# Performance work log

Hardware: AMD Instinct MI355X
Metric: run time of the kernel (lower is better)

## Reference

```python
import jax, jax.numpy as jnp
import numpy as np

IN_CHANNELS = 128
N_NODES = 100000
N_EDGES = 625000


def setup_inputs() -> dict:
    key = jax.random.key(0)
    k1, k2, k3, k4, k5, k6 = jax.random.split(key, 6)
    d = IN_CHANNELS
    x = jax.random.normal(k1, (N_NODES, d), dtype=jnp.float32)
    edge_index = jax.random.randint(k2, (2, N_EDGES), 0, N_NODES, dtype=jnp.int64)
    # Linear params, torch default init: U(-1/sqrt(fan_in), 1/sqrt(fan_in))
    b1_bound = 1.0 / np.sqrt(2 * d)
    W1 = jax.random.uniform(k3, (d, 2 * d), minval=-b1_bound, maxval=b1_bound, dtype=jnp.float32)
    b1 = jax.random.uniform(k4, (d,), minval=-b1_bound, maxval=b1_bound, dtype=jnp.float32)
    b2_bound = 1.0 / np.sqrt(d)
    W2 = jax.random.uniform(k5, (1, d), minval=-b2_bound, maxval=b2_bound, dtype=jnp.float32)
    b2 = jax.random.uniform(k6, (1,), minval=-b2_bound, maxval=b2_bound, dtype=jnp.float32)
    return {"x": x, "edge_index": edge_index, "W1": W1, "b1": b1, "W2": W2, "b2": b2}


def reference(x, edge_index, W1, b1, W2, b2):
    # Gather endpoint features and concat along feature dim: [E, 2d]
    h = jnp.concatenate([x[edge_index[0]], x[edge_index[1]]], axis=1)
    h = jax.nn.relu(h @ W1.T + b1)          # [E, d]
    h = jax.nn.relu(h @ W2.T + b2)          # [E, 1]
    return jax.nn.sigmoid(h)
```

## Files before the change

### kernel.cpp

```cpp
#include <hip/hip_runtime.h>
#include <hip/hip_bf16.h>
#include <hip/hip_fp16.h>
#include <math.h>


typedef short    s16x4 __attribute__((ext_vector_type(4)));
typedef short    s16x8 __attribute__((ext_vector_type(8)));
typedef float    f32x4 __attribute__((ext_vector_type(4)));
typedef _Float16 h16x2 __attribute__((ext_vector_type(2)));

#define D    128
#define ALD  136

static __device__ inline short f2bf(float f) {
    unsigned u = __builtin_bit_cast(unsigned, f);
    unsigned r = (u + 0x7FFFu + ((u >> 16) & 1u)) >> 16;
    return (short)r;
}

static __device__ inline unsigned enc1_sw(float f) {
    f = fminf(fmaxf(f, -448.f), 448.f);
    unsigned short h = __builtin_bit_cast(unsigned short, (_Float16)(f * (1.0f / 256.0f)));
    unsigned s = (h >> 8) & 0x80u;
    unsigned mag = h & 0x7FFFu;
    mag = mag + 0x3Fu + ((mag >> 7) & 1u);
    return s | ((mag >> 7) & 0x7Fu);
}
static __device__ inline unsigned enc2(float a, float b) {
#if __has_builtin(__builtin_amdgcn_cvt_pk_fp8_f32)
    return ((unsigned)__builtin_amdgcn_cvt_pk_fp8_f32(a, b, 0, false)) & 0xFFFFu;
#else
    return enc1_sw(a) | (enc1_sw(b) << 8);
#endif
}

#if __has_builtin(__builtin_amdgcn_cvt_pk_f16_fp8)
#define YSC 1.0f
static __device__ inline h16x2 dec2lo(unsigned v) {
    return __builtin_amdgcn_cvt_pk_f16_fp8((short)v);
}
static __device__ inline h16x2 dec2hi(unsigned v) {
    return __builtin_amdgcn_cvt_pk_f16_fp8((short)(v >> 16));
}
#else
#define YSC 256.0f
static __device__ inline h16x2 dec2lo(unsigned v) {
    unsigned p = __builtin_amdgcn_perm(0u, v, 0x0C010C00u);
    unsigned h = ((p << 8) & 0x80008000u) | ((p << 7) & 0x3F803F80u);
    return __builtin_bit_cast(h16x2, h);
}
static __device__ inline h16x2 dec2hi(unsigned v) {
    unsigned p = __builtin_amdgcn_perm(0u, v, 0x0C030C02u);
    unsigned h = ((p << 8) & 0x80008000u) | ((p << 7) & 0x3F803F80u);
    return __builtin_bit_cast(h16x2, h);
}
#endif

static __device__ inline h16x2 reluh(h16x2 v) {
#if __has_builtin(__builtin_elementwise_max)
    h16x2 z = { (_Float16)0.0f, (_Float16)0.0f };
    return __builtin_elementwise_max(v, z);
#else
    unsigned u = __builtin_bit_cast(unsigned, v);
    unsigned m = ((u >> 15) & 0x00010001u) * 0xFFFFu;
    u &= ~m;
    return __builtin_bit_cast(h16x2, u);
#endif
}

static __device__ inline float dot2acc(h16x2 a, h16x2 b, float c) {
#if __has_builtin(__builtin_amdgcn_fdot2)
    return __builtin_amdgcn_fdot2(a, b, c, false);
#else
    return c + (float)a[0] * (float)b[0] + (float)a[1] * (float)b[1];
#endif
}

__global__ __launch_bounds__(256) void pack_w1_kernel(
    const float* __restrict__ W1, short* __restrict__ W1F)
{
    int g    = blockIdx.x * 256 + threadIdx.x;
    int lane = g & 63;
    int c    = (g >> 6) & 3;
    int j    = (g >> 8) & 3;
    int cs   = g >> 10;
    int o    = cs * 64 + j * 16 + (lane & 15);
    int kb   = c * 32 + (lane >> 4) * 8;
    const float* wp = W1 + (size_t)(o & 127) * 256 + (o >> 7) * 128 + kb;
    float4 u0 = *(const float4*)wp;
    float4 u1 = *(const float4*)(wp + 4);
    s16x8 v = { f2bf(u0.x), f2bf(u0.y), f2bf(u0.z), f2bf(u0.w),
                f2bf(u1.x), f2bf(u1.y), f2bf(u1.z), f2bf(u1.w) };
    *(s16x8*)&W1F[(size_t)g * 8] = v;
}

__global__ __launch_bounds__(256) void precompute_kernel(
    const float* __restrict__ x,
    const short* __restrict__ W1F,
    const float* __restrict__ b1,
    unsigned char* __restrict__ Y8,
    int N, int ntiles)
{
    __shared__ short At[2][32 * ALD];

    const int tid  = threadIdx.x;
    const int wid  = tid >> 6;
    const int lane = tid & 63;
    const int quad = lane >> 4, l15 = lane & 15;
    const int cs   = wid;

    s16x8 bf[4][4];
    #pragma unroll
    for (int j = 0; j < 4; ++j)
        #pragma unroll
        for (int c = 0; c < 4; ++c)
            bf[c][j] = *(const s16x8*)&W1F[(size_t)(((cs * 4 + j) * 4 + c) * 64 + lane) * 8];

    f32x4 b1v[4];
    #pragma unroll
    for (int j = 0; j < 4; ++j) {
        if (cs < 2) b1v[j] = *(const f32x4*)&b1[cs * 64 + j * 16 + quad * 4];
        else        b1v[j] = (f32x4){0.f, 0.f, 0.f, 0.f};
    }

    const int srow = tid >> 3;
    const int sc0  = (tid & 7) * 4;
    const int g    = gridDim.x;

    int t = blockIdx.x;
    float4 xv[4];
    {
        int m = t * 32 + srow; if (m >= N) m = N - 1;
        const float* xp = &x[(size_t)m * D + sc0];
        #pragma unroll
        for (int p = 0; p < 4; ++p)
            xv[p] = *(const float4*)(xp + p * 32);
    }
    #pragma unroll
    for (int p = 0; p < 4; ++p) {
        s16x4 bv = { f2bf(xv[p].x), f2bf(xv[p].y), f2bf(xv[p].z), f2bf(xv[p].w) };
        *(s16x4*)&At[0][srow * ALD + sc0 + p * 32] = bv;
    }
    __syncthreads();

    int buf = 0;
    while (t < ntiles) {
        const int tn = t + g;

        if (tn < ntiles) {
            int m = tn * 32 + srow; if (m >= N) m = N - 1;
            const float* xp = &x[(size_t)m * D + sc0];
            #pragma unroll
            for (int p = 0; p < 4; ++p)
                xv[p] = *(const float4*)(xp + p * 32);
        }

        f32x4 acc[2][4] = {};
        #pragma unroll
        for (int c = 0; c < 4; ++c) {
            s16x8 af[2];
            #pragma unroll
            for (int i = 0; i < 2; ++i)
                af[i] = *(const s16x8*)&At[buf][(i * 16 + l15) * ALD + c * 32 + quad * 8];
            #pragma unroll
            for (int i = 0; i < 2; ++i)
                #pragma unroll
                for (int j = 0; j < 4; ++j)
                    acc[i][j] = __builtin_amdgcn_mfma_f32_16x16x32_bf16(
                        bf[c][j], af[i], acc[i][j], 0, 0, 0);
        }

        const int m0 = t * 32;
        #pragma unroll
        for (int i = 0; i < 2; ++i) {
            int m = m0 + i * 16 + l15;
            if (m < N) {
                unsigned char* yp = Y8 + (size_t)m * 256 + cs * 64 + quad * 4;
                #pragma unroll
                for (int j = 0; j < 4; ++j) {
                    f32x4 v = acc[i][j] + b1v[j];
                    unsigned dw = enc2(v[0], v[1]) | (enc2(v[2], v[3]) << 16);
                    *(unsigned*)(yp + j * 16) = dw;
                }
            }
        }

        if (tn < ntiles) {
            #pragma unroll
            for (int p = 0; p < 4; ++p) {
                s16x4 bv = { f2bf(xv[p].x), f2bf(xv[p].y), f2bf(xv[p].z), f2bf(xv[p].w) };
                *(s16x4*)&At[buf ^ 1][srow * ALD + sc0 + p * 32] = bv;
            }
        }
        __syncthreads();
        buf ^= 1;
        t = tn;
    }
}

#define EPB 128

__global__ __launch_bounds__(256) void edge_kernel(
    const unsigned char* __restrict__ Y8,
    const int*           __restrict__ ei,
    const float*         __restrict__ W2,
    const float*         __restrict__ b2,
    float*               __restrict__ out,
    int E)
{
    const int tid = threadIdx.x;
    const int sub = tid & 7;
    const int grp = tid >> 3;
    const int e0  = blockIdx.x * EPB + grp;

    h16x2 w2h[8];
    {
        const float* wp = &W2[sub * 16];
        #pragma unroll
        for (int q = 0; q < 8; ++q) {
            float2 f = *(const float2*)(wp + q * 2);
            w2h[q] = (h16x2){ (_Float16)(f.x * YSC), (_Float16)(f.y * YSC) };
        }
    }

    int  ee[4]; bool vv[4]; uint4 L[4], R[4];
    #pragma unroll
    for (int k = 0; k < 4; ++k) {
        ee[k] = e0 + 32 * k;
        vv[k] = (ee[k] < E);
        int src = vv[k] ? ei[ee[k]] : 0;
        int dst = vv[k] ? ei[E + ee[k]] : 0;
        L[k] = *(const uint4*)(Y8 + (size_t)src * 256 + sub * 16);
        R[k] = *(const uint4*)(Y8 + (size_t)dst * 256 + 128 + sub * 16);
    }

    float s[4] = { 0.f, 0.f, 0.f, 0.f };
    #pragma unroll
    for (int k = 0; k < 4; ++k) {
        const unsigned* a = (const unsigned*)&L[k];
        const unsigned* c = (const unsigned*)&R[k];
        #pragma unroll
        for (int d = 0; d < 4; ++d) {
            h16x2 za = reluh(dec2lo(a[d]) + dec2lo(c[d]));
            s[k] = dot2acc(za, w2h[2*d],     s[k]);
            h16x2 zb = reluh(dec2hi(a[d]) + dec2hi(c[d]));
            s[k] = dot2acc(zb, w2h[2*d + 1], s[k]);
        }
    }

    #pragma unroll
    for (int k = 0; k < 4; ++k) {
        s[k] += __shfl_xor(s[k], 1);
        s[k] += __shfl_xor(s[k], 2);
        s[k] += __shfl_xor(s[k], 4);
    }

    if (sub == 0) {
        float bb = b2[0];
        #pragma unroll
        for (int k = 0; k < 4; ++k) {
            if (vv[k]) {
                float t = fmaxf(s[k] + bb, 0.f);
                out[ee[k]] = 1.0f / (1.0f + expf(-t));
            }
        }
    }
}

#define BM   128
#define BK   64
#define LDT  72

__global__ __launch_bounds__(256) void decoder_fallback_kernel(
    const float* __restrict__ x, const int* __restrict__ ei,
    const float* __restrict__ W1, const float* __restrict__ b1,
    const float* __restrict__ W2, const float* __restrict__ b2,
    float* __restrict__ out, int E)
{
    __shared__ int   nid[2][BM];
    __shared__ short At[BM * LDT];
    __shared__ short Bt[D * LDT];
    __shared__ float rowsum[BM][2];

    const int tid = threadIdx.x;
    const int e0  = blockIdx.x * BM;
    if (tid < BM) { int e = e0 + tid; nid[0][tid] = (e < E) ? ei[e] : 0; }
    else { int e = e0 + (tid - BM); nid[1][tid - BM] = (e < E) ? ei[E + e] : 0; }

    const int wid = tid >> 6, lane = tid & 63;
    const int wm = wid >> 1, wn = wid & 1;
    const int quad = lane >> 4, l15 = lane & 15;
    const int srow = tid >> 4, scol = (tid & 15) * 4;
    f32x4 acc[4][4] = {};
    __syncthreads();

    for (int t = 0; t < 4; ++t) {
        const int* ids = nid[t >> 1];
        const int kx = (t & 1) * BK, kw = t * BK;
        #pragma unroll
        for (int p = 0; p < 8; ++p) {
            int row = srow + p * 16;
            float4 v = *(const float4*)&x[(size_t)ids[row] * D + kx + scol];
            s16x4 bv = { f2bf(v.x), f2bf(v.y), f2bf(v.z), f2bf(v.w) };
            *(s16x4*)&At[row * LDT + scol] = bv;
        }
        #pragma unroll
        for (int p = 0; p < 8; ++p) {
            int n = srow + p * 16;
            float4 v = *(const float4*)&W1[n * 256 + kw + scol];
            s16x4 bv = { f2bf(v.x), f2bf(v.y), f2bf(v.z), f2bf(v.w) };
            *(s16x4*)&Bt[n * LDT + scol] = bv;
        }
        __syncthreads();
        #pragma unroll
        for (int c = 0; c < 2; ++c) {
            const int kc = c * 32;
            s16x8 af[4], bfr[4];
            #pragma unroll
            for (int i = 0; i < 4; ++i)
                af[i] = *(const s16x8*)&At[(wm*64 + i*16 + l15) * LDT + kc + quad*8];
            #pragma unroll
            for (int j = 0; j < 4; ++j)
                bfr[j] = *(const s16x8*)&Bt[(wn*64 + j*16 + l15) * LDT + kc + quad*8];
            #pragma unroll
            for (int i = 0; i < 4; ++i)
                #pragma unroll
                for (int j = 0; j < 4; ++j)
                    acc[i][j] = __builtin_amdgcn_mfma_f32_16x16x32_bf16(
                        af[i], bfr[j], acc[i][j], 0, 0, 0);
        }
        __syncthreads();
    }
    float b1v[4], w2v[4];
    #pragma unroll
    for (int j = 0; j < 4; ++j) {
        int col = wn*64 + j*16 + l15;
        b1v[j] = b1[col]; w2v[j] = W2[col];
    }
    float psum[16];
    #pragma unroll
    for (int t = 0; t < 16; ++t) psum[t] = 0.f;
    #pragma unroll
    for (int i = 0; i < 4; ++i)
        #pragma unroll
        for (int j = 0; j < 4; ++j)
            #pragma unroll
            for (int r = 0; r < 4; ++r) {
                float c = fmaxf(acc[i][j][r] + b1v[j], 0.f);
                psum[i*4 + r] += c * w2v[j];
            }
    #pragma unroll
    for (int off = 1; off < 16; off <<= 1)
        #pragma unroll
        for (int t = 0; t < 16; ++t)
            psum[t] += __shfl_xor(psum[t], off);
    if (l15 == 0) {
        #pragma unroll
        for (int i = 0; i < 4; ++i)
            #pragma unroll
            for (int r = 0; r < 4; ++r)
                rowsum[wm*64 + i*16 + quad*4 + r][wn] = psum[i*4 + r];
    }
    __syncthreads();
    if (tid < BM) {
        int e = e0 + tid;
        if (e < E) {
            float s = rowsum[tid][0] + rowsum[tid][1] + b2[0];
            s = fmaxf(s, 0.f);
            out[e] = 1.0f / (1.0f + expf(-s));
        }
    }
}

extern "C" void kernel_launch(void* const* d_in, const int* in_sizes, int n_in,
                              void* d_out, int out_size, void* d_ws, size_t ws_size,
                              hipStream_t stream) {
    const float* x  = (const float*)d_in[0];
    const int*   ei = (const int*)d_in[1];
    const float* W1 = (const float*)d_in[2];
    const float* b1 = (const float*)d_in[3];
    const float* W2 = (const float*)d_in[4];
    const float* b2 = (const float*)d_in[5];
    float* out = (float*)d_out;

    int E = in_sizes[1] / 2;
    int N = in_sizes[0] / D;

    size_t y_bytes = (size_t)N * 256;
    size_t need    = y_bytes + 32768 * sizeof(short);
    if (ws_size >= need) {
        unsigned char* Y8  = (unsigned char*)d_ws;
        short*         W1F = (short*)((char*)d_ws + y_bytes);
        pack_w1_kernel<<<16, 256, 0, stream>>>(W1, W1F);
        int ntiles = (N + 31) / 32;
        int gridA  = (ntiles + 3) / 4;
        precompute_kernel<<<gridA, 256, 0, stream>>>(x, W1F, b1, Y8, N, ntiles);
        int gridB = (E + EPB - 1) / EPB;
        edge_kernel<<<gridB, 256, 0, stream>>>(Y8, ei, W2, b2, out, E);
    } else {
        int nblocks = (E + BM - 1) / BM;
        decoder_fallback_kernel<<<nblocks, 256, 0, stream>>>(
            x, ei, W1, b1, W2, b2, out, E);
    }
}
```

Before: 140.5 us.

## Stage x tiles via direct global-to-LDS loads and drop W1 pack kernel

Removes the separate W1 packing kernel; each block now converts W1 to bf16 fragments itself. The x tile is staged as fp32 straight into swizzled LDS with global_load_lds and converted to bf16 with packed cvt instructions when fragments are read. The grid becomes a fixed persistent size with an occupancy hint, and the bias is folded into the accumulator init. Y8 stores are widened to 16-byte writes using lane shuffles. Costs: every block rereads and converts W1, LDS use doubles because tiles stay fp32, and the kernel now relies on inline asm for bf16 conversion.

```diff
diff --git a/kernel.cpp b/kernel.cpp
--- a/kernel.cpp
+++ b/kernel.cpp
@@ -7,15 +7,27 @@
 typedef short    s16x4 __attribute__((ext_vector_type(4)));
 typedef short    s16x8 __attribute__((ext_vector_type(8)));
 typedef float    f32x4 __attribute__((ext_vector_type(4)));
+typedef unsigned u32x4 __attribute__((ext_vector_type(4)));
 typedef _Float16 h16x2 __attribute__((ext_vector_type(2)));
 
-#define D    128
-#define ALD  136
+#define D 128
 
 static __device__ inline short f2bf(float f) {
     unsigned u = __builtin_bit_cast(unsigned, f);
     unsigned r = (u + 0x7FFFu + ((u >> 16) & 1u)) >> 16;
     return (short)r;
+}
+
+static __device__ inline unsigned pkbf16(float a, float b) {
+    unsigned r;
+    asm("v_cvt_pk_bf16_f32 %0, %1, %2" : "=v"(r) : "v"(a), "v"(b));
+    return r;
+}
+
+static __device__ inline void stage16(const void* g, void* l) {
+    __builtin_amdgcn_global_load_lds(
+        (const __attribute__((address_space(1))) void*)g,
+        (__attribute__((address_space(3))) void*)l, 16, 0, 0);
 }
 
 static __device__ inline unsigned enc1_sw(float f) {
@@ -76,32 +88,16 @@
 #endif
 }
 
-__global__ __launch_bounds__(256) void pack_w1_kernel(
-    const float* __restrict__ W1, short* __restrict__ W1F)
-{
-    int g    = blockIdx.x * 256 + threadIdx.x;
-    int lane = g & 63;
-    int c    = (g >> 6) & 3;
-    int j    = (g >> 8) & 3;
-    int cs   = g >> 10;
-    int o    = cs * 64 + j * 16 + (lane & 15);
-    int kb   = c * 32 + (lane >> 4) * 8;
-    const float* wp = W1 + (size_t)(o & 127) * 256 + (o >> 7) * 128 + kb;
-    float4 u0 = *(const float4*)wp;
-    float4 u1 = *(const float4*)(wp + 4);
-    s16x8 v = { f2bf(u0.x), f2bf(u0.y), f2bf(u0.z), f2bf(u0.w),
-                f2bf(u1.x), f2bf(u1.y), f2bf(u1.z), f2bf(u1.w) };
-    *(s16x8*)&W1F[(size_t)g * 8] = v;
-}
-
-__global__ __launch_bounds__(256) void precompute_kernel(
+#define GRIDA 768
+
+__global__ __launch_bounds__(256, 3) void precompute_kernel(
     const float* __restrict__ x,
-    const short* __restrict__ W1F,
+    const float* __restrict__ W1,
     const float* __restrict__ b1,
     unsigned char* __restrict__ Y8,
     int N, int ntiles)
 {
-    __shared__ short At[2][32 * ALD];
+    __shared__ float Xt[2][32 * 128];
 
     const int tid  = threadIdx.x;
     const int wid  = tid >> 6;
@@ -111,88 +107,117 @@
 
     s16x8 bf[4][4];
     #pragma unroll
-    for (int j = 0; j < 4; ++j)
-        #pragma unroll
-        for (int c = 0; c < 4; ++c)
-            bf[c][j] = *(const s16x8*)&W1F[(size_t)(((cs * 4 + j) * 4 + c) * 64 + lane) * 8];
-
-    f32x4 b1v[4];
-    #pragma unroll
     for (int j = 0; j < 4; ++j) {
-        if (cs < 2) b1v[j] = *(const f32x4*)&b1[cs * 64 + j * 16 + quad * 4];
-        else        b1v[j] = (f32x4){0.f, 0.f, 0.f, 0.f};
-    }
-
-    const int srow = tid >> 3;
-    const int sc0  = (tid & 7) * 4;
-    const int g    = gridDim.x;
+        #pragma unroll
+        for (int c = 0; c < 4; ++c) {
+            int o  = cs * 64 + j * 16 + l15;
+            int kb = c * 32 + quad * 8;
+            const float* wp = W1 + (size_t)(o & 127) * 256 + (o >> 7) * 128 + kb;
+            float4 u0 = *(const float4*)wp;
+            float4 u1 = *(const float4*)(wp + 4);
+            bf[c][j] = (s16x8){ f2bf(u0.x), f2bf(u0.y), f2bf(u0.z), f2bf(u0.w),
+                                f2bf(u1.x), f2bf(u1.y), f2bf(u1.z), f2bf(u1.w) };
+        }
+    }
+
+    const int rl   = wid * 2 + (lane >> 5);
+    const int colb = (lane & 31) * 16;
+    const char* xbytes = (const char*)x;
+
+    auto stage_tile = [&](int tt, int bb) {
+        char* lb = (char*)&Xt[bb][0] + wid * 1024;
+        #pragma unroll
+        for (int i = 0; i < 4; ++i) {
+            int row = i * 8 + rl;
+            int m = tt * 32 + row; if (m >= N) m = N - 1;
+            stage16(xbytes + (size_t)m * 512 + (colb ^ ((row & 7) << 4)),
+                    lb + i * 4096);
+        }
+    };
 
     int t = blockIdx.x;
-    float4 xv[4];
-    {
-        int m = t * 32 + srow; if (m >= N) m = N - 1;
-        const float* xp = &x[(size_t)m * D + sc0];
-        #pragma unroll
-        for (int p = 0; p < 4; ++p)
-            xv[p] = *(const float4*)(xp + p * 32);
-    }
-    #pragma unroll
-    for (int p = 0; p < 4; ++p) {
-        s16x4 bv = { f2bf(xv[p].x), f2bf(xv[p].y), f2bf(xv[p].z), f2bf(xv[p].w) };
-        *(s16x4*)&At[0][srow * ALD + sc0 + p * 32] = bv;
-    }
-    __syncthreads();
-
+    if (t < ntiles) stage_tile(t, 0);
+
+    const int swz = (l15 & 7) << 4;
     int buf = 0;
     while (t < ntiles) {
-        const int tn = t + g;
-
-        if (tn < ntiles) {
-            int m = tn * 32 + srow; if (m >= N) m = N - 1;
-            const float* xp = &x[(size_t)m * D + sc0];
-            #pragma unroll
-            for (int p = 0; p < 4; ++p)
-                xv[p] = *(const float4*)(xp + p * 32);
-        }
-
-        f32x4 acc[2][4] = {};
-        #pragma unroll
-        for (int c = 0; c < 4; ++c) {
-            s16x8 af[2];
-            #pragma unroll
-            for (int i = 0; i < 2; ++i)
-                af[i] = *(const s16x8*)&At[buf][(i * 16 + l15) * ALD + c * 32 + quad * 8];
-            #pragma unroll
-            for (int i = 0; i < 2; ++i)
+        const int tn = t + GRIDA;
+
+        asm volatile("s_waitcnt vmcnt(0)" ::: "memory");
+        __syncthreads();
+
+        f32x4 acc[2][4];
+        #pragma unroll
+        for (int j = 0; j < 4; ++j) {
+            f32x4 bi = (cs < 2) ? *(const f32x4*)&b1[cs * 64 + j * 16 + quad * 4]
+                                : (f32x4){0.f, 0.f, 0.f, 0.f};
+            acc[0][j] = bi; acc[1][j] = bi;
+        }
+
+        s16x8 af[2][4];
+        {
+            const char* xb8 = (const char*)&Xt[buf][0];
+            #pragma unroll
+            for (int i2 = 0; i2 < 2; ++i2) {
+                const char* rp = xb8 + (i2 * 16 + l15) * 512;
+                #pragma unroll
+                for (int c = 0; c < 4; ++c) {
+                    int kb = c * 128 + quad * 32;
+                    f32x4 lo = *(const f32x4*)(rp + ( kb       ^ swz));
+                    f32x4 hi = *(const f32x4*)(rp + ((kb + 16) ^ swz));
+                    u32x4 pk;
+                    pk[0] = pkbf16(lo[0], lo[1]);
+                    pk[1] = pkbf16(lo[2], lo[3]);
+                    pk[2] = pkbf16(hi[0], hi[1]);
+                    pk[3] = pkbf16(hi[2], hi[3]);
+                    af[i2][c] = __builtin_bit_cast(s16x8, pk);
+                }
+            }
+        }
+
+        if (tn < ntiles) stage_tile(tn, buf ^ 1);
+
+        #pragma unroll
+        for (int c = 0; c < 4; ++c)
+            #pragma unroll
+            for (int i2 = 0; i2 < 2; ++i2)
                 #pragma unroll
                 for (int j = 0; j < 4; ++j)
-                    acc[i][j] = __builtin_amdgcn_mfma_f32_16x16x32_bf16(
-                        bf[c][j], af[i], acc[i][j], 0, 0, 0);
-        }
+                    acc[i2][j] = __builtin_amdgcn_mfma_f32_16x16x32_bf16(
+                        bf[c][j], af[i2][c], acc[i2][j], 0, 0, 0);
 
         const int m0 = t * 32;
-        #pragma unroll
-        for (int i = 0; i < 2; ++i) {
-            int m = m0 + i * 16 + l15;
-            if (m < N) {
-                unsigned char* yp = Y8 + (size_t)m * 256 + cs * 64 + quad * 4;
-                #pragma unroll
-                for (int j = 0; j < 4; ++j) {
-                    f32x4 v = acc[i][j] + b1v[j];
-                    unsigned dw = enc2(v[0], v[1]) | (enc2(v[2], v[3]) << 16);
-                    *(unsigned*)(yp + j * 16) = dw;
-                }
+        const bool qb0 = (quad & 1), qb1 = (quad & 2);
+        #pragma unroll
+        for (int i2 = 0; i2 < 2; ++i2) {
+            unsigned dw[4];
+            #pragma unroll
+            for (int j = 0; j < 4; ++j) {
+                f32x4 v = acc[i2][j];
+                dw[j] = enc2(v[0], v[1]) | (enc2(v[2], v[3]) << 16);
             }
-        }
-
-        if (tn < ntiles) {
-            #pragma unroll
-            for (int p = 0; p < 4; ++p) {
-                s16x4 bv = { f2bf(xv[p].x), f2bf(xv[p].y), f2bf(xv[p].z), f2bf(xv[p].w) };
-                *(s16x4*)&At[buf ^ 1][srow * ALD + sc0 + p * 32] = bv;
-            }
-        }
-        __syncthreads();
+            unsigned s01 = qb0 ? dw[0] : dw[1];
+            unsigned r01 = __shfl_xor(s01, 16);
+            unsigned s23 = qb0 ? dw[2] : dw[3];
+            unsigned r23 = __shfl_xor(s23, 16);
+            unsigned a0 = qb0 ? r01 : dw[0];
+            unsigned a1 = qb0 ? dw[1] : r01;
+            unsigned a2 = qb0 ? r23 : dw[2];
+            unsigned a3 = qb0 ? dw[3] : r23;
+            unsigned s02 = qb1 ? a0 : a2;
+            unsigned r02 = __shfl_xor(s02, 32);
+            unsigned s13 = qb1 ? a1 : a3;
+            unsigned r13 = __shfl_xor(s13, 32);
+            uint4 ov;
+            ov.x = qb1 ? r02 : a0;
+            ov.y = qb1 ? r13 : a1;
+            ov.z = qb1 ? a2 : r02;
+            ov.w = qb1 ? a3 : r13;
+            int m = m0 + i2 * 16 + l15;
+            if (m < N)
+                *(uint4*)(Y8 + (size_t)m * 256 + cs * 64 + quad * 16) = ov;
+        }
+
         buf ^= 1;
         t = tn;
     }
@@ -387,14 +412,11 @@
     int N = in_sizes[0] / D;
 
     size_t y_bytes = (size_t)N * 256;
-    size_t need    = y_bytes + 32768 * sizeof(short);
-    if (ws_size >= need) {
-        unsigned char* Y8  = (unsigned char*)d_ws;
-        short*         W1F = (short*)((char*)d_ws + y_bytes);
-        pack_w1_kernel<<<16, 256, 0, stream>>>(W1, W1F);
+    if (ws_size >= y_bytes) {
+        unsigned char* Y8 = (unsigned char*)d_ws;
         int ntiles = (N + 31) / 32;
-        int gridA  = (ntiles + 3) / 4;
-        precompute_kernel<<<gridA, 256, 0, stream>>>(x, W1F, b1, Y8, N, ntiles);
+        int gridA  = (ntiles < GRIDA) ? ntiles : GRIDA;
+        precompute_kernel<<<gridA, 256, 0, stream>>>(x, W1, b1, Y8, N, ntiles);
         int gridB = (E + EPB - 1) / EPB;
         edge_kernel<<<gridB, 256, 0, stream>>>(Y8, ei, W2, b2, out, E);
     } else {
```

Result: no change. 137.8 us (-1.9%).
